# Kernel optimization log

Measured on AMD Instinct MI355X. Metric: run time of the kernel, lower is better.

## Reference

```python
import jax, jax.numpy as jnp
import numpy as np

N_NODES = 100000
N_RELS = 3
N_EDGES = 300000


def setup_inputs() -> dict:
    key = jax.random.key(0)
    ks = jax.random.split(key, 6)
    x = jax.random.normal(ks[0], (N_NODES, 128), dtype=jnp.float32)
    W1 = jax.random.normal(ks[1], (N_RELS, 128, 128), dtype=jnp.float32) * (128 ** -0.5)
    b1 = jnp.zeros((N_RELS, 128), dtype=jnp.float32)
    W2 = jax.random.normal(ks[2], (N_RELS, 128, 64), dtype=jnp.float32) * (128 ** -0.5)
    b2 = jnp.zeros((N_RELS, 64), dtype=jnp.float32)
    edges = jax.random.randint(ks[3], (N_RELS, 2, N_EDGES), 0, N_NODES, dtype=jnp.int64)
    return {"x": x, "W1": W1, "b1": b1, "W2": W2, "b2": b2, "edges": edges}


def _hetero_graphconv_layer(x, W, b, edges, n_nodes):
    """Sum over relations of GraphConv(norm='both'):
    y_r = D_in^{-1/2} A_r (D_out^{-1/2} x) W_r + b_r   (degrees clamped to >=1, DGL default).
    HeteroGraphConv default aggregate is 'sum'."""
    out = jnp.zeros((n_nodes, W.shape[-1]), dtype=x.dtype)
    ones = jnp.ones((edges.shape[-1],), dtype=x.dtype)
    for r in range(edges.shape[0]):  # small fixed loop over relation types
        src, dst = edges[r, 0], edges[r, 1]
        out_deg = jnp.clip(jax.ops.segment_sum(ones, src, num_segments=n_nodes), 1.0)
        in_deg = jnp.clip(jax.ops.segment_sum(ones, dst, num_segments=n_nodes), 1.0)
        # transform scaled source features, then sparse aggregate to destinations
        m = (x * (out_deg ** -0.5)[:, None]) @ W[r]          # [N, out_f]
        agg = jax.ops.segment_sum(m[src], dst, num_segments=n_nodes)  # SpMM via gather+scatter
        out = out + agg * (in_deg ** -0.5)[:, None] + b[r]
    return out


def reference(x, W1, b1, W2, b2, edges):
    n = x.shape[0]
    h = jax.nn.relu(_hetero_graphconv_layer(x, W1, b1, edges, n))
    h = jax.nn.relu(_hetero_graphconv_layer(h, W2, b2, edges, n))
    return h
```

## Files before the change

### kernel.cpp

```cpp
#include <hip/hip_runtime.h>
#include <hip/hip_bf16.h>
#include <stdint.h>


constexpr int TPB = 256;

typedef __attribute__((ext_vector_type(8))) short short8;
typedef __attribute__((ext_vector_type(4))) float f32x4;

__device__ __forceinline__ float bf2f(unsigned short u) {
    return __uint_as_float(((unsigned)u) << 16);
}
__device__ __forceinline__ unsigned short f2bf(float f) {
    return __bfloat16_as_ushort(__float2bfloat16(f));
}


__global__ void count_kernel(const int* __restrict__ edges, unsigned* __restrict__ cnt,
                             int total, int E, int N) {
    int i = blockIdx.x * blockDim.x + threadIdx.x;
    if (i >= total) return;
    atomicAdd(&cnt[(size_t)(i / E) * N + edges[i]], 1u);
}

__global__ __launch_bounds__(256) void scan_local_kernel(const unsigned* __restrict__ cnt,
                                                         int* __restrict__ off,
                                                         unsigned* __restrict__ bsum,
                                                         int N, int nb) {
    int r = blockIdx.x / nb, blk = blockIdx.x - r * nb;
    const unsigned* in = cnt + (size_t)(2 * r + 1) * N;
    int* o = off + (size_t)r * (N + 1);
    const int t = threadIdx.x, lane = t & 63, wid = t >> 6;
    int base = blk * 1024 + t * 4;
    unsigned v0 = (base + 0 < N) ? in[base + 0] : 0u;
    unsigned v1 = (base + 1 < N) ? in[base + 1] : 0u;
    unsigned v2 = (base + 2 < N) ? in[base + 2] : 0u;
    unsigned v3 = (base + 3 < N) ? in[base + 3] : 0u;
    unsigned p1 = v0, p2 = p1 + v1, p3 = p2 + v2, tt = p3 + v3;
    unsigned x = tt;
#pragma unroll
    for (int d = 1; d < 64; d <<= 1) {
        unsigned tmp = __shfl_up(x, d, 64);
        if (lane >= d) x += tmp;
    }
    __shared__ unsigned ws4[4];
    if (lane == 63) ws4[wid] = x;
    __syncthreads();
    unsigned woff = 0;
#pragma unroll
    for (int w2 = 0; w2 < 4; ++w2)
        if (w2 < wid) woff += ws4[w2];
    unsigned excl = woff + x - tt;
    if (base + 0 < N) o[base + 0] = (int)excl;
    if (base + 1 < N) o[base + 1] = (int)(excl + p1);
    if (base + 2 < N) o[base + 2] = (int)(excl + p2);
    if (base + 3 < N) o[base + 3] = (int)(excl + p3);
    if (t == 255) bsum[r * nb + blk] = woff + x;
}

__global__ __launch_bounds__(128) void scan_bsum_kernel(unsigned* __restrict__ bsum,
                                                        int* __restrict__ off,
                                                        int nb, int N, int E) {
    const int t = threadIdx.x, lane = t & 63, wid = t >> 6;
    __shared__ unsigned wtot[2];
    for (int r = 0; r < 3; ++r) {
        unsigned v = (t < nb) ? bsum[r * nb + t] : 0u;
        unsigned x = v;
#pragma unroll
        for (int d = 1; d < 64; d <<= 1) {
            unsigned tmp = __shfl_up(x, d, 64);
            if (lane >= d) x += tmp;
        }
        if (lane == 63) wtot[wid] = x;
        __syncthreads();
        unsigned add = (wid == 1) ? wtot[0] : 0u;
        if (t < nb) bsum[r * nb + t] = add + x - v;
        if (t == 0) off[(size_t)r * (N + 1) + N] = E;
        __syncthreads();
    }
}

__global__ void finalize_off_kernel(int* __restrict__ off, const unsigned* __restrict__ bsum,
                                    int* __restrict__ cur, int N, int nb) {
    int i = blockIdx.x * blockDim.x + threadIdx.x;
    if (i >= 3 * N) return;
    int r = i / N, n = i - r * N;
    int v = off[(size_t)r * (N + 1) + n] + (int)bsum[r * nb + (n >> 10)];
    off[(size_t)r * (N + 1) + n] = v;
    cur[i] = v;
}

__global__ void fill_kernel(const int* __restrict__ edges, int* __restrict__ cur,
                            int* __restrict__ csr_src, int E, int N) {
    int gid = blockIdx.x * blockDim.x + threadIdx.x;
    if (gid >= 3 * E) return;
    int r = gid / E, e = gid - r * E;
    int d  = edges[(size_t)(2 * r + 1) * E + e];
    int sv = edges[(size_t)(2 * r) * E + e];
    int pos = atomicAdd(&cur[(size_t)r * N + d], 1);
    csr_src[(size_t)r * E + pos] = sv;
}

__global__ void scale_inplace_kernel(unsigned* __restrict__ buf, int total) {
    int i = blockIdx.x * blockDim.x + threadIdx.x;
    if (i >= total) return;
    unsigned c = buf[i];
    ((float*)buf)[i] = rsqrtf((float)(c ? c : 1u));
}


template <typename XT>
__global__ __launch_bounds__(256) void mfma_gemm_kernel(const XT* __restrict__ X,
                                                        const float* __restrict__ W,
                                                        int WS, int c0,
                                                        __hip_bfloat16* __restrict__ T, int N) {
    __shared__ short bs[8192];
    const int t = threadIdx.x;
    const int lane = t & 63, wv = t >> 6;
    const int m0 = blockIdx.x * 64;

#pragma unroll
    for (int i = 0; i < 8; ++i) {
        int linear = i * 256 + t;
        int cc = linear & 63, r4 = linear >> 6;
        int r = r4 << 2;
        const float* wp = W + (size_t)r * WS + c0 + cc;
        unsigned u0 = f2bf(wp[0]);
        unsigned u1 = f2bf(wp[WS]);
        unsigned u2 = f2bf(wp[2 * WS]);
        unsigned u3 = f2bf(wp[3 * WS]);
        int kk = r4 >> 3, jg = (r4 >> 1) & 3, j0 = (r4 & 1) * 4;
        int l = jg * 16 + (cc & 15), c = cc >> 4;
        int slot = (((kk << 2) | c) << 9) + l * 8 + j0;
        *reinterpret_cast<uint2*>(&bs[slot]) = make_uint2(u0 | (u1 << 16), u2 | (u3 << 16));
    }

    const int row = m0 + wv * 16 + (lane & 15);
    const bool ok = row < N;
    short8 a[4];
    if constexpr (sizeof(XT) == 4) {
        const float* xr = (const float*)X + (size_t)row * 128 + ((lane >> 4) << 3);
#pragma unroll
        for (int kk = 0; kk < 4; ++kk) {
            short8 av = {};
            if (ok) {
                float4 f0 = *reinterpret_cast<const float4*>(xr + kk * 32);
                float4 f1 = *reinterpret_cast<const float4*>(xr + kk * 32 + 4);
                av[0] = (short)f2bf(f0.x); av[1] = (short)f2bf(f0.y);
                av[2] = (short)f2bf(f0.z); av[3] = (short)f2bf(f0.w);
                av[4] = (short)f2bf(f1.x); av[5] = (short)f2bf(f1.y);
                av[6] = (short)f2bf(f1.z); av[7] = (short)f2bf(f1.w);
            }
            a[kk] = av;
        }
    } else {
        const short* xr = (const short*)X + (size_t)row * 128 + ((lane >> 4) << 3);
#pragma unroll
        for (int kk = 0; kk < 4; ++kk) {
            short8 av = {};
            if (ok) av = *reinterpret_cast<const short8*>(xr + kk * 32);
            a[kk] = av;
        }
    }

    __syncthreads();

    f32x4 acc4[4] = {{0.f, 0.f, 0.f, 0.f}, {0.f, 0.f, 0.f, 0.f},
                     {0.f, 0.f, 0.f, 0.f}, {0.f, 0.f, 0.f, 0.f}};
#pragma unroll
    for (int c = 0; c < 4; ++c) {
#pragma unroll
        for (int kk = 0; kk < 4; ++kk) {
            short8 b = *reinterpret_cast<const short8*>(&bs[(((kk << 2) | c) << 9) + lane * 8]);
            acc4[c] = __builtin_amdgcn_mfma_f32_16x16x32_bf16(a[kk], b, acc4[c], 0, 0, 0);
        }
    }

#pragma unroll
    for (int c = 0; c < 4; ++c) {
        int gcol = c * 16 + (lane & 15);
#pragma unroll
        for (int q = 0; q < 4; ++q) {
            int grow = m0 + wv * 16 + ((lane >> 4) << 2) + q;
            if (grow < N) T[(size_t)grow * 64 + gcol] = __float2bfloat16(acc4[c][q]);
        }
    }
}


template <int PHASE>
__global__ __launch_bounds__(256) void gather_kernel(const int* __restrict__ off,
                                                     const int* __restrict__ csr_src,
                                                     const __hip_bfloat16* __restrict__ T,
                                                     const float* __restrict__ s_out,
                                                     const float* __restrict__ s_in,
                                                     float* __restrict__ acc,
                                                     const float* __restrict__ b, int FT, int c0,
                                                     __hip_bfloat16* __restrict__ h, int N) {
    int gid = blockIdx.x * blockDim.x + threadIdx.x;
    int n = gid >> 4;
    if (n >= N) return;
    int j = (gid & 15) << 2;
    int e0 = off[n], e1 = off[n + 1];
    float sx = 0.f, sy = 0.f, sz = 0.f, sw = 0.f;
    for (int e = e0; e < e1; ++e) {
        int sN = csr_src[e];
        float w = s_out[sN];
        ushort4 raw = *reinterpret_cast<const ushort4*>(&T[(size_t)sN * 64 + j]);
        sx += w * bf2f(raw.x);
        sy += w * bf2f(raw.y);
        sz += w * bf2f(raw.z);
        sw += w * bf2f(raw.w);
    }
    float si = s_in[n];
    float4* p = reinterpret_cast<float4*>(&acc[(size_t)n * 64 + j]);
    if constexpr (PHASE == 0) {
        int bj = c0 + j;
        float4 o;
        o.x = b[bj + 0] + b[FT + bj + 0] + b[2 * FT + bj + 0] + sx * si;
        o.y = b[bj + 1] + b[FT + bj + 1] + b[2 * FT + bj + 1] + sy * si;
        o.z = b[bj + 2] + b[FT + bj + 2] + b[2 * FT + bj + 2] + sz * si;
        o.w = b[bj + 3] + b[FT + bj + 3] + b[2 * FT + bj + 3] + sw * si;
        *p = o;
    } else if constexpr (PHASE == 1) {
        float4 v = *p;
        v.x += sx * si; v.y += sy * si; v.z += sz * si; v.w += sw * si;
        *p = v;
    } else if constexpr (PHASE == 2) {
        float4 v = *p;
        ushort4 o;
        o.x = f2bf(fmaxf(v.x + sx * si, 0.f));
        o.y = f2bf(fmaxf(v.y + sy * si, 0.f));
        o.z = f2bf(fmaxf(v.z + sz * si, 0.f));
        o.w = f2bf(fmaxf(v.w + sw * si, 0.f));
        *reinterpret_cast<ushort4*>(&h[(size_t)n * 128 + c0 + j]) = o;
    } else {
        float4 v = *p;
        v.x = fmaxf(v.x + sx * si, 0.f);
        v.y = fmaxf(v.y + sy * si, 0.f);
        v.z = fmaxf(v.z + sz * si, 0.f);
        v.w = fmaxf(v.w + sw * si, 0.f);
        *p = v;
    }
}

static inline int cdiv(int a, int b) { return (a + b - 1) / b; }

extern "C" void kernel_launch(void* const* d_in, const int* in_sizes, int n_in,
                              void* d_out, int out_size, void* d_ws, size_t ws_size,
                              hipStream_t stream) {
    const float* x  = (const float*)d_in[0];
    const float* W1 = (const float*)d_in[1];
    const float* b1 = (const float*)d_in[2];
    const float* W2 = (const float*)d_in[3];
    const float* b2 = (const float*)d_in[4];
    const int*   edges = (const int*)d_in[5];
    float* out = (float*)d_out;

    const int N = in_sizes[0] / 128;
    const int E = in_sizes[5] / 6;
    const int nb = cdiv(N, 1024);

    auto align256 = [](char* p) { return (char*)(((uintptr_t)p + 255) & ~(uintptr_t)255); };
    char* w = (char*)d_ws;
    unsigned* cnt = (unsigned*)w;
    float* s = (float*)w;                       w = align256(w + (size_t)6 * N * 4);
    __hip_bfloat16* h = (__hip_bfloat16*)w;     w = align256(w + (size_t)N * 128 * 2);
    __hip_bfloat16* T = (__hip_bfloat16*)w;     w = align256(w + (size_t)N * 64 * 2);
    int* off = (int*)w;                         w = align256(w + (size_t)3 * (N + 1) * 4);
    int* cur = (int*)w;                         w = align256(w + (size_t)3 * N * 4);
    int* csr = (int*)w;                         w = align256(w + (size_t)3 * E * 4);
    unsigned* bsum = (unsigned*)w;

    hipMemsetAsync(cnt, 0, (size_t)6 * N * 4, stream);
    count_kernel<<<cdiv(6 * E, TPB), TPB, 0, stream>>>(edges, cnt, 6 * E, E, N);
    scan_local_kernel<<<3 * nb, 256, 0, stream>>>(cnt, off, bsum, N, nb);
    scan_bsum_kernel<<<1, 128, 0, stream>>>(bsum, off, nb, N, E);
    finalize_off_kernel<<<cdiv(3 * N, TPB), TPB, 0, stream>>>(off, bsum, cur, N, nb);
    fill_kernel<<<cdiv(3 * E, TPB), TPB, 0, stream>>>(edges, cur, csr, E, N);
    scale_inplace_kernel<<<cdiv(6 * N, TPB), TPB, 0, stream>>>(cnt, 6 * N);

    const int ggrid = cdiv(N * 16, TPB);
    const int mgrid = cdiv(N, 64);

    for (int c0 = 0; c0 < 128; c0 += 64) {
        for (int r = 0; r < 3; ++r) {
            mfma_gemm_kernel<float><<<mgrid, 256, 0, stream>>>(
                x, W1 + (size_t)r * 128 * 128, 128, c0, T, N);
            const int* offr = off + (size_t)r * (N + 1);
            const int* csrr = csr + (size_t)r * E;
            const float* so = s + (size_t)(2 * r) * N;
            const float* si = s + (size_t)(2 * r + 1) * N;
            if (r == 0)
                gather_kernel<0><<<ggrid, TPB, 0, stream>>>(offr, csrr, T, so, si, out, b1, 128, c0, h, N);
            else if (r == 1)
                gather_kernel<1><<<ggrid, TPB, 0, stream>>>(offr, csrr, T, so, si, out, b1, 128, c0, h, N);
            else
                gather_kernel<2><<<ggrid, TPB, 0, stream>>>(offr, csrr, T, so, si, out, b1, 128, c0, h, N);
        }
    }

    for (int r = 0; r < 3; ++r) {
        mfma_gemm_kernel<__hip_bfloat16><<<mgrid, 256, 0, stream>>>(
            h, W2 + (size_t)r * 128 * 64, 64, 0, T, N);
        const int* offr = off + (size_t)r * (N + 1);
        const int* csrr = csr + (size_t)r * E;
        const float* so = s + (size_t)(2 * r) * N;
        const float* si = s + (size_t)(2 * r + 1) * N;
        if (r == 0)
            gather_kernel<0><<<ggrid, TPB, 0, stream>>>(offr, csrr, T, so, si, out, b2, 64, 0, h, N);
        else if (r == 1)
            gather_kernel<1><<<ggrid, TPB, 0, stream>>>(offr, csrr, T, so, si, out, b2, 64, 0, h, N);
        else
            gather_kernel<3><<<ggrid, TPB, 0, stream>>>(offr, csrr, T, so, si, out, b2, 64, 0, h, N);
    }
}
```

Measured before the change: 536.7 us.

## Fuse three relations per GEMM and gather launch, drop fp32 accumulator round-trips

The GEMM kernel now computes the transforms for all three relations in one launch, writing three T buffers. The gather kernel walks all three relations' CSR lists per node, so the sum, bias and ReLU finish in registers instead of round-tripping through a float accumulator in global memory. This cuts kernel launches, re-reads of X, and acc read/write traffic. In exchange T grows threefold (workspace is reused for cur/bsum, with a 32-column fallback when space is short), and LDS use and register pressure per block rise.

```diff
diff --git a/kernel.cpp b/kernel.cpp
--- a/kernel.cpp
+++ b/kernel.cpp
@@ -109,29 +109,32 @@
 }
 
 
-template <typename XT>
-__global__ __launch_bounds__(256) void mfma_gemm_kernel(const XT* __restrict__ X,
-                                                        const float* __restrict__ W,
-                                                        int WS, int c0,
-                                                        __hip_bfloat16* __restrict__ T, int N) {
-    __shared__ short bs[8192];
+template <int CH, typename XT>
+__global__ __launch_bounds__(256) void mfma_gemm3_kernel(const XT* __restrict__ X,
+                                                         const float* __restrict__ W,
+                                                         int WS, int c0,
+                                                         __hip_bfloat16* __restrict__ T, int N) {
+    constexpr int CT = CH / 16;
+    constexpr int FR = 4 * CT;
+    __shared__ short bs[3 * FR * 512];
     const int t = threadIdx.x;
     const int lane = t & 63, wv = t >> 6;
     const int m0 = blockIdx.x * 64;
 
-#pragma unroll
-    for (int i = 0; i < 8; ++i) {
-        int linear = i * 256 + t;
-        int cc = linear & 63, r4 = linear >> 6;
+    constexpr int TOT = 3 * 32 * CH;
+    for (int linear = t; linear < TOT; linear += 256) {
+        int rrel = linear / (32 * CH);
+        int rem = linear - rrel * (32 * CH);
+        int r4 = rem / CH, cc = rem - r4 * CH;
         int r = r4 << 2;
-        const float* wp = W + (size_t)r * WS + c0 + cc;
+        const float* wp = W + (size_t)rrel * 128 * WS + (size_t)r * WS + c0 + cc;
         unsigned u0 = f2bf(wp[0]);
         unsigned u1 = f2bf(wp[WS]);
         unsigned u2 = f2bf(wp[2 * WS]);
         unsigned u3 = f2bf(wp[3 * WS]);
         int kk = r4 >> 3, jg = (r4 >> 1) & 3, j0 = (r4 & 1) * 4;
         int l = jg * 16 + (cc & 15), c = cc >> 4;
-        int slot = (((kk << 2) | c) << 9) + l * 8 + j0;
+        int slot = ((rrel * FR + kk * CT + c) << 9) + l * 8 + j0;
         *reinterpret_cast<uint2*>(&bs[slot]) = make_uint2(u0 | (u1 << 16), u2 | (u3 << 16));
     }
 
@@ -165,86 +168,136 @@
 
     __syncthreads();
 
-    f32x4 acc4[4] = {{0.f, 0.f, 0.f, 0.f}, {0.f, 0.f, 0.f, 0.f},
-                     {0.f, 0.f, 0.f, 0.f}, {0.f, 0.f, 0.f, 0.f}};
-#pragma unroll
-    for (int c = 0; c < 4; ++c) {
-#pragma unroll
-        for (int kk = 0; kk < 4; ++kk) {
-            short8 b = *reinterpret_cast<const short8*>(&bs[(((kk << 2) | c) << 9) + lane * 8]);
-            acc4[c] = __builtin_amdgcn_mfma_f32_16x16x32_bf16(a[kk], b, acc4[c], 0, 0, 0);
-        }
-    }
-
-#pragma unroll
-    for (int c = 0; c < 4; ++c) {
-        int gcol = c * 16 + (lane & 15);
-#pragma unroll
-        for (int q = 0; q < 4; ++q) {
-            int grow = m0 + wv * 16 + ((lane >> 4) << 2) + q;
-            if (grow < N) T[(size_t)grow * 64 + gcol] = __float2bfloat16(acc4[c][q]);
-        }
-    }
-}
-
-
-template <int PHASE>
-__global__ __launch_bounds__(256) void gather_kernel(const int* __restrict__ off,
-                                                     const int* __restrict__ csr_src,
-                                                     const __hip_bfloat16* __restrict__ T,
-                                                     const float* __restrict__ s_out,
-                                                     const float* __restrict__ s_in,
-                                                     float* __restrict__ acc,
-                                                     const float* __restrict__ b, int FT, int c0,
-                                                     __hip_bfloat16* __restrict__ h, int N) {
+    f32x4 acc4[3 * CT];
+#pragma unroll
+    for (int f = 0; f < 3 * CT; ++f) acc4[f] = {0.f, 0.f, 0.f, 0.f};
+#pragma unroll
+    for (int rrel = 0; rrel < 3; ++rrel) {
+#pragma unroll
+        for (int c = 0; c < CT; ++c) {
+#pragma unroll
+            for (int kk = 0; kk < 4; ++kk) {
+                short8 b = *reinterpret_cast<const short8*>(
+                    &bs[((rrel * FR + kk * CT + c) << 9) + lane * 8]);
+                acc4[rrel * CT + c] =
+                    __builtin_amdgcn_mfma_f32_16x16x32_bf16(a[kk], b, acc4[rrel * CT + c], 0, 0, 0);
+            }
+        }
+    }
+
+#pragma unroll
+    for (int rrel = 0; rrel < 3; ++rrel) {
+        __hip_bfloat16* Tr = T + (size_t)rrel * N * CH;
+#pragma unroll
+        for (int c = 0; c < CT; ++c) {
+            int gcol = c * 16 + (lane & 15);
+            f32x4 v = acc4[rrel * CT + c];
+#pragma unroll
+            for (int q = 0; q < 4; ++q) {
+                int grow = m0 + wv * 16 + ((lane >> 4) << 2) + q;
+                if (grow < N) Tr[(size_t)grow * CH + gcol] = __float2bfloat16(v[q]);
+            }
+        }
+    }
+}
+
+
+template <int CH, int PHASE>
+__global__ __launch_bounds__(256) void gather3_kernel(const int* __restrict__ off,
+                                                      const int* __restrict__ csr,
+                                                      const __hip_bfloat16* __restrict__ T,
+                                                      const float* __restrict__ s,
+                                                      const float* __restrict__ b, int FT, int c0,
+                                                      float* __restrict__ outp,
+                                                      __hip_bfloat16* __restrict__ h,
+                                                      int N, int E) {
+    constexpr int LPN = CH / 4;
     int gid = blockIdx.x * blockDim.x + threadIdx.x;
-    int n = gid >> 4;
+    int n = gid / LPN;
     if (n >= N) return;
-    int j = (gid & 15) << 2;
-    int e0 = off[n], e1 = off[n + 1];
-    float sx = 0.f, sy = 0.f, sz = 0.f, sw = 0.f;
-    for (int e = e0; e < e1; ++e) {
-        int sN = csr_src[e];
-        float w = s_out[sN];
-        ushort4 raw = *reinterpret_cast<const ushort4*>(&T[(size_t)sN * 64 + j]);
-        sx += w * bf2f(raw.x);
-        sy += w * bf2f(raw.y);
-        sz += w * bf2f(raw.z);
-        sw += w * bf2f(raw.w);
-    }
-    float si = s_in[n];
-    float4* p = reinterpret_cast<float4*>(&acc[(size_t)n * 64 + j]);
+    int j = (gid % LPN) * 4;
+    int bj = c0 + j;
+    float ox = b[bj + 0] + b[FT + bj + 0] + b[2 * FT + bj + 0];
+    float oy = b[bj + 1] + b[FT + bj + 1] + b[2 * FT + bj + 1];
+    float oz = b[bj + 2] + b[FT + bj + 2] + b[2 * FT + bj + 2];
+    float ow = b[bj + 3] + b[FT + bj + 3] + b[2 * FT + bj + 3];
+#pragma unroll
+    for (int r = 0; r < 3; ++r) {
+        const int* offr = off + (size_t)r * (N + 1);
+        const int* csrr = csr + (size_t)r * E;
+        const float* s_out = s + (size_t)(2 * r) * N;
+        const __hip_bfloat16* Tr = T + (size_t)r * N * CH;
+        int e0 = offr[n], e1 = offr[n + 1];
+        float sx = 0.f, sy = 0.f, sz = 0.f, sw = 0.f;
+        for (int e = e0; e < e1; ++e) {
+            int sN = csrr[e];
+            float w = s_out[sN];
+            ushort4 raw = *reinterpret_cast<const ushort4*>(&Tr[(size_t)sN * CH + j]);
+            sx += w * bf2f(raw.x);
+            sy += w * bf2f(raw.y);
+            sz += w * bf2f(raw.z);
+            sw += w * bf2f(raw.w);
+        }
+        float si = s[(size_t)(2 * r + 1) * N + n];
+        ox += si * sx; oy += si * sy; oz += si * sz; ow += si * sw;
+    }
     if constexpr (PHASE == 0) {
-        int bj = c0 + j;
-        float4 o;
-        o.x = b[bj + 0] + b[FT + bj + 0] + b[2 * FT + bj + 0] + sx * si;
-        o.y = b[bj + 1] + b[FT + bj + 1] + b[2 * FT + bj + 1] + sy * si;
-        o.z = b[bj + 2] + b[FT + bj + 2] + b[2 * FT + bj + 2] + sz * si;
-        o.w = b[bj + 3] + b[FT + bj + 3] + b[2 * FT + bj + 3] + sw * si;
-        *p = o;
-    } else if constexpr (PHASE == 1) {
-        float4 v = *p;
-        v.x += sx * si; v.y += sy * si; v.z += sz * si; v.w += sw * si;
-        *p = v;
-    } else if constexpr (PHASE == 2) {
-        float4 v = *p;
         ushort4 o;
-        o.x = f2bf(fmaxf(v.x + sx * si, 0.f));
-        o.y = f2bf(fmaxf(v.y + sy * si, 0.f));
-        o.z = f2bf(fmaxf(v.z + sz * si, 0.f));
-        o.w = f2bf(fmaxf(v.w + sw * si, 0.f));
+        o.x = f2bf(fmaxf(ox, 0.f));
+        o.y = f2bf(fmaxf(oy, 0.f));
+        o.z = f2bf(fmaxf(oz, 0.f));
+        o.w = f2bf(fmaxf(ow, 0.f));
         *reinterpret_cast<ushort4*>(&h[(size_t)n * 128 + c0 + j]) = o;
     } else {
-        float4 v = *p;
-        v.x = fmaxf(v.x + sx * si, 0.f);
-        v.y = fmaxf(v.y + sy * si, 0.f);
-        v.z = fmaxf(v.z + sz * si, 0.f);
-        v.w = fmaxf(v.w + sw * si, 0.f);
-        *p = v;
+        float4 o;
+        o.x = fmaxf(ox, 0.f);
+        o.y = fmaxf(oy, 0.f);
+        o.z = fmaxf(oz, 0.f);
+        o.w = fmaxf(ow, 0.f);
+        *reinterpret_cast<float4*>(&outp[(size_t)n * 64 + c0 + j]) = o;
     }
 }
 
 static inline int cdiv(int a, int b) { return (a + b - 1) / b; }
+
+template <int CH>
+static void run_pipeline(const float* x, const float* W1, const float* b1,
+                         const float* W2, const float* b2, const int* edges,
+                         float* out, void* d_ws, int N, int E, hipStream_t stream) {
+    const int nb = cdiv(N, 1024);
+    auto align256 = [](char* p) { return (char*)(((uintptr_t)p + 255) & ~(uintptr_t)255); };
+    char* w = (char*)d_ws;
+    unsigned* cnt = (unsigned*)w;
+    float* s = (float*)w;                       w = align256(w + (size_t)6 * N * 4);
+    __hip_bfloat16* h = (__hip_bfloat16*)w;     w = align256(w + (size_t)N * 128 * 2);
+    __hip_bfloat16* T = (__hip_bfloat16*)w;     w = align256(w + (size_t)3 * N * CH * 2);
+    int* off = (int*)w;                         w = align256(w + (size_t)3 * (N + 1) * 4);
+    int* csr = (int*)w;
+    int* cur = (int*)T;
+    unsigned* bsum = (unsigned*)((char*)T + (size_t)3 * N * 4 + 256);
+
+    hipMemsetAsync(cnt, 0, (size_t)6 * N * 4, stream);
+    count_kernel<<<cdiv(6 * E, TPB), TPB, 0, stream>>>(edges, cnt, 6 * E, E, N);
+    scan_local_kernel<<<3 * nb, 256, 0, stream>>>(cnt, off, bsum, N, nb);
+    scan_bsum_kernel<<<1, 128, 0, stream>>>(bsum, off, nb, N, E);
+    finalize_off_kernel<<<cdiv(3 * N, TPB), TPB, 0, stream>>>(off, bsum, cur, N, nb);
+    fill_kernel<<<cdiv(3 * E, TPB), TPB, 0, stream>>>(edges, cur, csr, E, N);
+    scale_inplace_kernel<<<cdiv(6 * N, TPB), TPB, 0, stream>>>(cnt, 6 * N);
+
+    const int mgrid = cdiv(N, 64);
+    const int ggrid = cdiv(N * (CH / 4), TPB);
+
+    for (int c0 = 0; c0 < 128; c0 += CH) {
+        mfma_gemm3_kernel<CH, float><<<mgrid, 256, 0, stream>>>(x, W1, 128, c0, T, N);
+        gather3_kernel<CH, 0><<<ggrid, TPB, 0, stream>>>(off, csr, T, s, b1, 128, c0,
+                                                         nullptr, h, N, E);
+    }
+    for (int c0 = 0; c0 < 64; c0 += CH) {
+        mfma_gemm3_kernel<CH, __hip_bfloat16><<<mgrid, 256, 0, stream>>>(h, W2, 64, c0, T, N);
+        gather3_kernel<CH, 1><<<ggrid, TPB, 0, stream>>>(off, csr, T, s, b2, 64, c0,
+                                                         out, nullptr, N, E);
+    }
+}
 
 extern "C" void kernel_launch(void* const* d_in, const int* in_sizes, int n_in,
                               void* d_out, int out_size, void* d_ws, size_t ws_size,
@@ -259,59 +312,11 @@
 
     const int N = in_sizes[0] / 128;
     const int E = in_sizes[5] / 6;
-    const int nb = cdiv(N, 1024);
-
-    auto align256 = [](char* p) { return (char*)(((uintptr_t)p + 255) & ~(uintptr_t)255); };
-    char* w = (char*)d_ws;
-    unsigned* cnt = (unsigned*)w;
-    float* s = (float*)w;                       w = align256(w + (size_t)6 * N * 4);
-    __hip_bfloat16* h = (__hip_bfloat16*)w;     w = align256(w + (size_t)N * 128 * 2);
-    __hip_bfloat16* T = (__hip_bfloat16*)w;     w = align256(w + (size_t)N * 64 * 2);
-    int* off = (int*)w;                         w = align256(w + (size_t)3 * (N + 1) * 4);
-    int* cur = (int*)w;                         w = align256(w + (size_t)3 * N * 4);
-    int* csr = (int*)w;                         w = align256(w + (size_t)3 * E * 4);
-    unsigned* bsum = (unsigned*)w;
-
-    hipMemsetAsync(cnt, 0, (size_t)6 * N * 4, stream);
-    count_kernel<<<cdiv(6 * E, TPB), TPB, 0, stream>>>(edges, cnt, 6 * E, E, N);
-    scan_local_kernel<<<3 * nb, 256, 0, stream>>>(cnt, off, bsum, N, nb);
-    scan_bsum_kernel<<<1, 128, 0, stream>>>(bsum, off, nb, N, E);
-    finalize_off_kernel<<<cdiv(3 * N, TPB), TPB, 0, stream>>>(off, bsum, cur, N, nb);
-    fill_kernel<<<cdiv(3 * E, TPB), TPB, 0, stream>>>(edges, cur, csr, E, N);
-    scale_inplace_kernel<<<cdiv(6 * N, TPB), TPB, 0, stream>>>(cnt, 6 * N);
-
-    const int ggrid = cdiv(N * 16, TPB);
-    const int mgrid = cdiv(N, 64);
-
-    for (int c0 = 0; c0 < 128; c0 += 64) {
-        for (int r = 0; r < 3; ++r) {
-            mfma_gemm_kernel<float><<<mgrid, 256, 0, stream>>>(
-                x, W1 + (size_t)r * 128 * 128, 128, c0, T, N);
-            const int* offr = off + (size_t)r * (N + 1);
-            const int* csrr = csr + (size_t)r * E;
-            const float* so = s + (size_t)(2 * r) * N;
-            const float* si = s + (size_t)(2 * r + 1) * N;
-            if (r == 0)
-                gather_kernel<0><<<ggrid, TPB, 0, stream>>>(offr, csrr, T, so, si, out, b1, 128, c0, h, N);
-            else if (r == 1)
-                gather_kernel<1><<<ggrid, TPB, 0, stream>>>(offr, csrr, T, so, si, out, b1, 128, c0, h, N);
-            else
-                gather_kernel<2><<<ggrid, TPB, 0, stream>>>(offr, csrr, T, so, si, out, b1, 128, c0, h, N);
-        }
-    }
-
-    for (int r = 0; r < 3; ++r) {
-        mfma_gemm_kernel<__hip_bfloat16><<<mgrid, 256, 0, stream>>>(
-            h, W2 + (size_t)r * 128 * 64, 64, 0, T, N);
-        const int* offr = off + (size_t)r * (N + 1);
-        const int* csrr = csr + (size_t)r * E;
-        const float* so = s + (size_t)(2 * r) * N;
-        const float* si = s + (size_t)(2 * r + 1) * N;
-        if (r == 0)
-            gather_kernel<0><<<ggrid, TPB, 0, stream>>>(offr, csrr, T, so, si, out, b2, 64, 0, h, N);
-        else if (r == 1)
-            gather_kernel<1><<<ggrid, TPB, 0, stream>>>(offr, csrr, T, so, si, out, b2, 64, 0, h, N);
-        else
-            gather_kernel<3><<<ggrid, TPB, 0, stream>>>(offr, csrr, T, so, si, out, b2, 64, 0, h, N);
-    }
-}
+
+    const size_t need64 = (size_t)6 * N * 4 + (size_t)N * 128 * 2 + (size_t)3 * N * 64 * 2 +
+                          (size_t)3 * (N + 1) * 4 + (size_t)3 * E * 4 + 4096;
+    if (ws_size >= need64)
+        run_pipeline<64>(x, W1, b1, W2, b2, edges, out, d_ws, N, E, stream);
+    else
+        run_pipeline<32>(x, W1, b1, W2, b2, edges, out, d_ws, N, E, stream);
+}
```

Result: faster. 495.9 us (-7.6%).
